# Kernel optimization log

Hardware: AMD Instinct MI355X
Metric: run time of the kernel (lower is better)

The kernel has to match this reference:

```python
import jax, jax.numpy as jnp
import numpy as np

V, E, H, B, P, Q = 100000, 300, 256, 64, 400, 50
NEG = -1e7


def _gru_param(k, s=0.08):
    k1, k2, k3, k4 = jax.random.split(k, 4)
    return (jax.random.normal(k1, (2, 3 * H, E)) * s,
            jax.random.normal(k2, (2, 3 * H, H)) * s,
            jax.random.normal(k3, (2, 3 * H)) * s,
            jax.random.normal(k4, (2, 3 * H)) * s)


def setup_inputs() -> dict:
    key = jax.random.key(0)
    ks = jax.random.split(key, 10)
    emb = (jax.random.normal(ks[0], (V, E)) * 0.1).at[0].set(0.0)  # padding_idx=0 row zeroed
    passage = jax.random.randint(ks[1], (B, P), 1, V)
    question = jax.random.randint(ks[2], (B, Q), 1, V)
    # variable lengths, padding (token 0) at the tail like pack_padded_sequence assumes
    p_len = 200 + (jnp.arange(B) * 7) % (P - 200)
    q_len = 20 + (jnp.arange(B) * 3) % (Q - 20)
    passage = jnp.where(jnp.arange(P)[None, :] < p_len[:, None], passage, 0)
    question = jnp.where(jnp.arange(Q)[None, :] < q_len[:, None], question, 0)
    pW_ih, pW_hh, pb_ih, pb_hh = _gru_param(ks[3])
    qW_ih, qW_hh, qb_ih, qb_hh = _gru_param(ks[4])
    start_w = jax.random.normal(ks[5], (6 * H,)) * 0.05
    start_b = jax.random.normal(ks[6], ()) * 0.05
    end_w = jax.random.normal(ks[7], (6 * H,)) * 0.05
    end_b = jax.random.normal(ks[8], ()) * 0.05
    return dict(passage=passage, question=question, emb=emb,
                pW_ih=pW_ih, pW_hh=pW_hh, pb_ih=pb_ih, pb_hh=pb_hh,
                qW_ih=qW_ih, qW_hh=qW_hh, qb_ih=qb_ih, qb_hh=qb_hh,
                start_w=start_w, start_b=start_b, end_w=end_w, end_b=end_b)


def bi_gru(x, mask, Wih, Whh, bih, bhh):
    """Bidirectional GRU with packed-sequence-equivalent masking.
    x: (B,T,E), mask: (B,T) float. Returns (B,T,2H). Padded outputs are 0,
    and the backward pass starts at the true last token (mask freezes state)."""
    m = mask[..., None]                                          # (B,T,1)
    xproj = jnp.einsum('bte,dhe->dbth', x, Wih) + bih[:, None, None, :]  # (2,B,T,3H)

    def run(xp, mm, Whh_d, bhh_d):
        def step(h, inp):
            xt, mt = inp                                         # (B,3H),(B,1)
            hp = h @ Whh_d.T + bhh_d
            r = jax.nn.sigmoid(xt[:, :H] + hp[:, :H])
            z = jax.nn.sigmoid(xt[:, H:2 * H] + hp[:, H:2 * H])
            n = jnp.tanh(xt[:, 2 * H:] + r * hp[:, 2 * H:])
            h_new = (1 - z) * n + z * h
            h_new = mt * h_new + (1 - mt) * h
            return h_new, h_new * mt
        h0 = jnp.zeros((xp.shape[0], H), xp.dtype)
        _, out = jax.lax.scan(step, h0, (xp.transpose(1, 0, 2), mm.transpose(1, 0, 2)))
        return out.transpose(1, 0, 2)                            # (B,T,H)

    fwd = run(xproj[0], m, Whh[0], bhh[0])
    bwd = run(xproj[1][:, ::-1], m[:, ::-1], Whh[1], bhh[1])[:, ::-1]
    return jnp.concatenate([fwd, bwd], axis=-1)


def reference(passage, question, emb,
              pW_ih, pW_hh, pb_ih, pb_hh,
              qW_ih, qW_hh, qb_ih, qb_hh,
              start_w, start_b, end_w, end_b):
    p_mask = (passage != 0).astype(jnp.float32)                  # (B,P)
    q_mask = (question != 0).astype(jnp.float32)                 # (B,Q)
    Hp = bi_gru(emb[passage], p_mask, pW_ih, pW_hh, pb_ih, pb_hh)  # (B,P,2H)
    Hq = bi_gru(emb[question], q_mask, qW_ih, qW_hh, qb_ih, qb_hh)  # (B,Q,2H)

    # Trilinear attention: decompose Linear over the cat([p, q, p*q]) terms
    w1, w2, w3 = start_w[:2 * H], start_w[2 * H:4 * H], start_w[4 * H:]
    scores = (Hp @ w1)[:, :, None] + (Hq @ w2)[:, None, :] \
        + jnp.einsum('bpd,bqd->bpq', Hp * w3, Hq) + start_b      # (B,P,Q)

    # allennlp masked_softmax: softmax(vector*mask) * mask, renormalized
    a = jax.nn.softmax(scores * q_mask[:, None, :], axis=-1) * q_mask[:, None, :]
    a = a / (a.sum(axis=-1, keepdims=True) + 1e-13)

    wavg = jnp.einsum('bpq,bqd->bpd', a, Hq)                     # (B,P,2H)
    combined = jnp.concatenate([Hp, wavg, Hp * wavg], axis=-1)   # (B,P,6H)

    start_logits = jnp.where(p_mask > 0, combined @ start_w + start_b, NEG)
    end_logits = jnp.where(p_mask > 0, combined @ end_w + end_b, NEG)
    log_mask = jnp.log(p_mask + 1e-45)
    softmax_start = jax.nn.log_softmax(start_logits + log_mask, axis=-1)
    softmax_end = jax.nn.log_softmax(end_logits + log_mask, axis=-1)
    return start_logits, end_logits, softmax_start, softmax_end
```

## Files before the change

### kernel.cpp

```cpp
#include <hip/hip_runtime.h>
#include <math.h>

constexpr int Bb = 64;
constexpr int Pp = 400;
constexpr int Qq = 50;
constexpr int Ee = 300;
constexpr int Hh = 256;
constexpr int H3 = 768;
constexpr int Dd = 512;

#define NEGC (-10000000.0f)
#define LOGTINY (-103.278929903f)

typedef _Float16 h2 __attribute__((ext_vector_type(2)));
typedef _Float16 f16x8 __attribute__((ext_vector_type(8)));
typedef float f32x4 __attribute__((ext_vector_type(4)));

__device__ __forceinline__ float allred(float v){
  #pragma unroll
  for (int off = 1; off < 64; off <<= 1) v += __shfl_xor(v, off);
  return v;
}
__device__ __forceinline__ float allmax(float v){
  #pragma unroll
  for (int off = 1; off < 64; off <<= 1) v = fmaxf(v, __shfl_xor(v, off));
  return v;
}
__device__ __forceinline__ float sigm(float x){ return 1.f / (1.f + expf(-x)); }

__device__ __forceinline__ float dot2f(unsigned a, unsigned b, float c){
#if __has_builtin(__builtin_amdgcn_fdot2)
  return __builtin_amdgcn_fdot2(__builtin_bit_cast(h2, a), __builtin_bit_cast(h2, b), c, false);
#else
  float r = c;
  asm("v_dot2_f32_f16 %0, %1, %2, %0" : "+v"(r) : "v"(a), "v"(b));
  return r;
#endif
}

#define U4C(v,c) ((c)==0?(v).x:((c)==1?(v).y:((c)==2?(v).z:(v).w)))

__global__ __launch_bounds__(256) void gather_a(const int* __restrict__ ptok,
                                                const int* __restrict__ qtok,
                                                const float* __restrict__ emb,
                                                _Float16* __restrict__ Agp,
                                                _Float16* __restrict__ Agq){
  int idx = blockIdx.x * 256 + threadIdx.x;
  if (idx >= (25600 + 3200) * 40) return;
  int ck = idx % 40;
  int row = idx / 40;
  int tokv; _Float16* dst;
  if (row < 25600){ tokv = ptok[row]; dst = Agp + (size_t)row * 320; }
  else { int r = row - 25600; tokv = qtok[r]; dst = Agq + (size_t)r * 320; }
  int c = ck * 8;
  const float* src = emb + (size_t)tokv * Ee;
  f16x8 v;
  #pragma unroll
  for (int i = 0; i < 8; ++i) v[i] = (c + i < Ee) ? (_Float16)src[c + i] : (_Float16)0.f;
  *(f16x8*)(dst + c) = v;
}

__global__ __launch_bounds__(256) void prep_wih16(const float* __restrict__ pW,
                                                  const float* __restrict__ qW,
                                                  _Float16* __restrict__ wih16){
  int idx = blockIdx.x * 256 + threadIdx.x;
  if (idx >= 2 * 2 * 768 * 160) return;
  int col2 = idx % 160;
  int r = idx / 160;
  int g = r / 1536;
  int dh = r % 1536;
  int c = col2 * 2;
  const float* W = g ? qW : pW;
  float2 v = make_float2(0.f, 0.f);
  if (c < Ee) v = *(const float2*)(W + (size_t)dh * Ee + c);
  h2 o = { (_Float16)v.x, (_Float16)v.y };
  *(h2*)(wih16 + (size_t)r * 320 + c) = o;
}

__global__ __launch_bounds__(256) void prep_w16(const float* __restrict__ pW,
                                                const float* __restrict__ qW,
                                                unsigned* __restrict__ w16){
  int idx = blockIdx.x * 256 + threadIdx.x;
  if (idx >= 393216) return;
  int c = idx & 3;
  int t = (idx >> 2) & 1023;
  int B = idx >> 12;
  int gd, g, ql;
  if (B < 28){
    gd = B / 7; int rb = B % 7;
    ql = rb / 3; g = rb % 3;
  } else if (B < 64){
    int lb0 = B - 28; gd = lb0 / 9; int lb = lb0 % 9;
    if (lb < 2){ ql = 2; g = lb + 1; }
    else if (lb < 8){ int v = lb - 2; ql = 3 + v / 3; g = v % 3; }
    else { ql = 5; g = 0; }
  } else {
    int sb0 = B - 64; gd = sb0 / 8; int sb = sb0 % 8;
    if (sb < 2){ ql = 5; g = sb + 1; }
    else { int v = sb - 2; ql = 6 + v / 3; g = v % 3; }
  }
  int j = t & 255, qq = t >> 8;
  int p = qq * 32 + ql * 4 + c;
  int row = g * 256 + j;
  int d = gd & 1, kind = gd >> 1;
  const float* W = kind ? qW : pW;
  const float* src = W + ((size_t)d * H3 + row) * Hh + 2 * p;
  _Float16 a = (_Float16)src[0], bb = (_Float16)src[1];
  unsigned short ua, ub;
  __builtin_memcpy(&ua, &a, 2); __builtin_memcpy(&ub, &bb, 2);
  w16[idx] = (unsigned)ua | ((unsigned)ub << 16);
}

__global__ __launch_bounds__(512) void xproj_mfma(const int* __restrict__ tok,
                                                  const _Float16* __restrict__ Ag,
                                                  const _Float16* __restrict__ wih16,
                                                  const float* __restrict__ bih,
                                                  _Float16* __restrict__ xp, int T){
  __shared__ __align__(16) _Float16 Af[128][72];
  __shared__ __align__(16) _Float16 Bf[128][72];
  __shared__ int anyflag;
  int tid = threadIdx.x;
  int m0 = blockIdx.y * 128;

  if (tid == 0) anyflag = 0;
  __syncthreads();
  if (tid < 128 && tok[m0 + tid] != 0) anyflag = 1;
  __syncthreads();
  if (!anyflag) return;

  int nt = blockIdx.x;
  int d = nt / 6, h0 = (nt % 6) * 128;
  int wid = tid >> 6, lane = tid & 63;
  int wr = wid >> 2, wc = wid & 3;

  int r0 = tid >> 3;
  int r1 = (tid + 512) >> 3;
  int cc = (tid & 7) * 8;
  const _Float16* eA0 = Ag + (size_t)(m0 + r0) * 320;
  const _Float16* eA1 = Ag + (size_t)(m0 + r1) * 320;
  const _Float16* wB0 = wih16 + ((size_t)d * H3 + h0 + r0) * 320;
  const _Float16* wB1 = wih16 + ((size_t)d * H3 + h0 + r1) * 320;

  f32x4 acc[4][2] = {};

  for (int k0 = 0; k0 < 320; k0 += 64){
    *(f16x8*)&Af[r0][cc] = *(const f16x8*)(eA0 + k0 + cc);
    *(f16x8*)&Af[r1][cc] = *(const f16x8*)(eA1 + k0 + cc);
    *(f16x8*)&Bf[r0][cc] = *(const f16x8*)(wB0 + k0 + cc);
    *(f16x8*)&Bf[r1][cc] = *(const f16x8*)(wB1 + k0 + cc);
    __syncthreads();
    #pragma unroll
    for (int kc = 0; kc < 2; ++kc){
      int kb = kc * 32 + (lane >> 4) * 8;
      f16x8 af[4], bf[2];
      #pragma unroll
      for (int i = 0; i < 4; ++i) af[i] = *(const f16x8*)&Af[wr * 64 + i * 16 + (lane & 15)][kb];
      #pragma unroll
      for (int jn = 0; jn < 2; ++jn) bf[jn] = *(const f16x8*)&Bf[wc * 32 + jn * 16 + (lane & 15)][kb];
      #pragma unroll
      for (int i = 0; i < 4; ++i)
        #pragma unroll
        for (int jn = 0; jn < 2; ++jn)
          acc[i][jn] = __builtin_amdgcn_mfma_f32_16x16x32_f16(af[i], bf[jn], acc[i][jn], 0, 0, 0);
    }
    __syncthreads();
  }

  #pragma unroll
  for (int jn = 0; jn < 2; ++jn){
    int h = h0 + wc * 32 + jn * 16 + (lane & 15);
    float bv = bih[d * H3 + h];
    #pragma unroll
    for (int i = 0; i < 4; ++i){
      #pragma unroll
      for (int r = 0; r < 4; ++r){
        int m = m0 + wr * 64 + i * 16 + (lane >> 4) * 4 + r;
        int bI = m / T, tI = m - bI * T;
        xp[(((size_t)d * Bb + bI) * T + tI) * H3 + h] = (_Float16)(acc[i][jn][r] + bv);
      }
    }
  }
}

__global__ __launch_bounds__(1024)
void gru_kernel(const int* __restrict__ ptok,
                const int* __restrict__ qtok,
                const _Float16* __restrict__ xpp,
                const _Float16* __restrict__ xpq,
                const unsigned* __restrict__ w16,
                const float* __restrict__ pbhh,
                const float* __restrict__ qbhh,
                float* __restrict__ Hp,
                float* __restrict__ Hq){
  int wg = blockIdx.x;
  bool isp = wg < 128;
  int lw = isp ? wg : wg - 128;
  int d = lw & 1, b = lw >> 1;
  int T = isp ? Pp : Qq;
  const int* tok = (isp ? ptok : qtok) + b * T;
  const _Float16* xrow = (isp ? xpp : xpq) + ((size_t)d * Bb + b) * T * H3;
  int gd = (isp ? 0 : 2) + d;
  const float* bhh = (isp ? pbhh : qbhh) + d * H3;
  float* Hout = (isp ? Hp : Hq) + (size_t)b * T * Dd + d * Hh;

  __shared__ __align__(16) uint4 ldsW[9 * 1024];
  __shared__ float part[3][3][Hh];
  __shared__ __align__(16) unsigned hbuf[2][128];

  int t = threadIdx.x;
  int j = t & 255, qq = t >> 8;
  const uint4* u4w = (const uint4*)w16;

  unsigned wrR[28];
  #pragma unroll
  for (int rb = 0; rb < 7; ++rb){
    uint4 v = u4w[((size_t)gd * 7 + rb) * 1024 + t];
    wrR[4 * rb + 0] = v.x; wrR[4 * rb + 1] = v.y; wrR[4 * rb + 2] = v.z; wrR[4 * rb + 3] = v.w;
  }
  #pragma unroll
  for (int i = 0; i < 28; ++i) asm volatile("" : "+v"(wrR[i]));

  #pragma unroll
  for (int lb = 0; lb < 9; ++lb)
    ldsW[lb * 1024 + t] = u4w[28 * 1024 + ((size_t)gd * 9 + lb) * 1024 + t];
  const uint4* wS = u4w + 64 * 1024 + (size_t)gd * 8 * 1024;

  float bh0 = bhh[j], bh1 = bhh[Hh + j], bh2 = bhh[2 * Hh + j];
  float h_old = 0.f;
  if (t < 128) hbuf[1][t] = 0u;
  __syncthreads();

  int t0 = d ? (T - 1) : 0;
  float pre0 = 0.f, pre1 = 0.f, pre2 = 0.f;
  if (qq == 0){
    pre0 = (float)xrow[(size_t)t0 * H3 + j];
    pre1 = (float)xrow[(size_t)t0 * H3 + Hh + j];
    pre2 = (float)xrow[(size_t)t0 * H3 + 2 * Hh + j];
  }

  for (int s = 0; s < T; ++s){
    int tt = d ? (T - 1 - s) : s;
    const uint4* hb4 = (const uint4*)&hbuf[(s + 1) & 1][qq * 32];
    float a0 = 0.f, a1 = 0.f, a2 = 0.f;

    uint4 sA0 = wS[0 * 1024 + t], sA1 = wS[1 * 1024 + t];
    uint4 sB0 = wS[2 * 1024 + t], sB1 = wS[3 * 1024 + t], sB2 = wS[4 * 1024 + t];
    uint4 sC0 = wS[5 * 1024 + t], sC1 = wS[6 * 1024 + t], sC2 = wS[7 * 1024 + t];

    #define DOT3(HQ, W0e, W1e, W2e) { _Pragma("unroll") \
      for (int c = 0; c < 4; ++c){ \
        unsigned hv = U4C(HQ, c); \
        a0 = dot2f(U4C(W0e, c), hv, a0); \
        a1 = dot2f(U4C(W1e, c), hv, a1); \
        a2 = dot2f(U4C(W2e, c), hv, a2); } }
    #define DOT1(HQ, W0e, ACC) { _Pragma("unroll") \
      for (int c = 0; c < 4; ++c){ \
        unsigned hv = U4C(HQ, c); \
        ACC = dot2f(U4C(W0e, c), hv, ACC); } }
    #define RQ(i) (*(const uint4*)&wrR[4 * (i)])

    uint4 h0q = hb4[0], h1q = hb4[1];
    DOT3(h0q, RQ(0), RQ(1), RQ(2))
    DOT3(h1q, RQ(3), RQ(4), RQ(5))
    uint4 h2q = hb4[2], h3q = hb4[3];
    DOT1(h2q, RQ(6), a0)
    { uint4 l1 = ldsW[0 * 1024 + t], l2 = ldsW[1 * 1024 + t];
      DOT1(h2q, l1, a1) DOT1(h2q, l2, a2) }
    { uint4 l0 = ldsW[2 * 1024 + t], l1 = ldsW[3 * 1024 + t], l2 = ldsW[4 * 1024 + t];
      DOT3(h3q, l0, l1, l2) }
    uint4 h4q = hb4[4], h5q = hb4[5];
    { uint4 l0 = ldsW[5 * 1024 + t], l1 = ldsW[6 * 1024 + t], l2 = ldsW[7 * 1024 + t];
      DOT3(h4q, l0, l1, l2) }
    { uint4 l0 = ldsW[8 * 1024 + t];
      DOT1(h5q, l0, a0) }
    DOT1(h5q, sA0, a1) DOT1(h5q, sA1, a2)
    uint4 h6q = hb4[6], h7q = hb4[7];
    DOT3(h6q, sB0, sB1, sB2)
    DOT3(h7q, sC0, sC1, sC2)
    #undef DOT3
    #undef DOT1
    #undef RQ

    if (qq != 0){
      part[qq - 1][0][j] = a0;
      part[qq - 1][1][j] = a1;
      part[qq - 1][2][j] = a2;
    }
    __syncthreads();
    if (qq == 0){
      float xt0 = pre0, xt1 = pre1, xt2 = pre2;
      if (s + 1 < T){
        int tn = d ? (T - 2 - s) : (s + 1);
        pre0 = (float)xrow[(size_t)tn * H3 + j];
        pre1 = (float)xrow[(size_t)tn * H3 + Hh + j];
        pre2 = (float)xrow[(size_t)tn * H3 + 2 * Hh + j];
      }
      float g0 = a0 + part[0][0][j] + part[1][0][j] + part[2][0][j] + bh0;
      float g1 = a1 + part[0][1][j] + part[1][1][j] + part[2][1][j] + bh1;
      float g2 = a2 + part[0][2][j] + part[1][2][j] + part[2][2][j] + bh2;
      float r = sigm(xt0 + g0);
      float z = sigm(xt1 + g1);
      float n = tanhf(xt2 + r * g2);
      float hnew = (1.f - z) * n + z * h_old;
      float m = (tok[tt] != 0) ? 1.f : 0.f;
      float hm = m * hnew + (1.f - m) * h_old;
      h_old = hm;
      ((_Float16*)hbuf[s & 1])[j] = (_Float16)hm;
      Hout[(size_t)tt * Dd + j] = hm * m;
    }
    __syncthreads();
  }
}

__global__ __launch_bounds__(512) void attn_kernel(const float* __restrict__ Hp,
                                                   const float* __restrict__ Hq,
                                                   const int* __restrict__ ptok,
                                                   const int* __restrict__ qtok,
                                                   const float* __restrict__ start_w,
                                                   const float* __restrict__ sbp,
                                                   const float* __restrict__ end_w,
                                                   const float* __restrict__ ebp,
                                                   float* __restrict__ out){
  extern __shared__ __align__(16) float lds[];
  float* hqs = lds;
  float* s2s = hqs + Qq * Dd;
  float* qms = s2s + 64;
  float* scw = qms + 64;
  float* aw  = scw + 512;

  int b = blockIdx.y, pc = blockIdx.x;
  int tid = threadIdx.x, wid = tid >> 6, lane = tid & 63;
  float sb = sbp[0], eb = ebp[0];

  float w1r[8], w2r[8], w3r[8], e1r[8], e2r[8], e3r[8];
  #pragma unroll
  for (int i = 0; i < 8; ++i){
    int c = lane * 8 + i;
    w1r[i] = start_w[c]; w2r[i] = start_w[Dd + c]; w3r[i] = start_w[2 * Dd + c];
    e1r[i] = end_w[c];   e2r[i] = end_w[Dd + c];   e3r[i] = end_w[2 * Dd + c];
  }
  for (int idx = tid; idx < Qq * Dd; idx += 512) hqs[idx] = Hq[(size_t)b * Qq * Dd + idx];
  __syncthreads();

  for (int q = wid; q < Qq; q += 8){
    float part = 0.f;
    const float* hq = hqs + q * Dd + lane * 8;
    #pragma unroll
    for (int i = 0; i < 8; ++i) part += hq[i] * w2r[i];
    part = allred(part);
    if (lane == 0){
      s2s[q] = part;
      qms[q] = (qtok[b * Qq + q] != 0) ? 1.f : 0.f;
    }
  }
  __syncthreads();

  for (int p = pc * 100 + wid; p < pc * 100 + 100; p += 8){
    const float* hprow = Hp + ((size_t)b * Pp + p) * Dd + lane * 8;
    float4 hv0 = *(const float4*)hprow;
    float4 hv1 = *(const float4*)(hprow + 4);
    float hpc[8] = {hv0.x, hv0.y, hv0.z, hv0.w, hv1.x, hv1.y, hv1.z, hv1.w};
    float hw3[8], he3[8];
    float s1 = 0.f, ed = 0.f;
    #pragma unroll
    for (int i = 0; i < 8; ++i){
      hw3[i] = hpc[i] * w3r[i];
      he3[i] = hpc[i] * e3r[i];
      s1 += hpc[i] * w1r[i];
      ed += hpc[i] * e1r[i];
    }
    #pragma unroll
    for (int off = 1; off < 64; off <<= 1){
      s1 += __shfl_xor(s1, off);
      ed += __shfl_xor(ed, off);
    }
    for (int q = 0; q < Qq; ++q){
      const float4* hq4 = (const float4*)(hqs + q * Dd + lane * 8);
      float4 a0 = hq4[0], a1 = hq4[1];
      float dot = hw3[0] * a0.x + hw3[1] * a0.y + hw3[2] * a0.z + hw3[3] * a0.w
                + hw3[4] * a1.x + hw3[5] * a1.y + hw3[6] * a1.z + hw3[7] * a1.w;
      dot = allred(dot);
      if (lane == 0) scw[wid * 64 + q] = (s1 + s2s[q] + dot + sb) * qms[q];
    }
    float v = (lane < Qq) ? scw[wid * 64 + lane] : -1e30f;
    float M = allmax(v);
    float ev = (lane < Qq) ? expf(v - M) : 0.f;
    float S = allred(ev);
    float am = (lane < Qq) ? (ev / S) * qms[lane] : 0.f;
    float Sm = allred(am);
    float af = am / (Sm + 1e-13f);
    if (lane < Qq) aw[wid * 64 + lane] = af;
    float wv[8] = {0.f, 0.f, 0.f, 0.f, 0.f, 0.f, 0.f, 0.f};
    for (int q = 0; q < Qq; ++q){
      float aq = aw[wid * 64 + q];
      const float4* hq4 = (const float4*)(hqs + q * Dd + lane * 8);
      float4 a0 = hq4[0], a1 = hq4[1];
      wv[0] += aq * a0.x; wv[1] += aq * a0.y; wv[2] += aq * a0.z; wv[3] += aq * a0.w;
      wv[4] += aq * a1.x; wv[5] += aq * a1.y; wv[6] += aq * a1.z; wv[7] += aq * a1.w;
    }
    float acc2 = 0.f, acc3 = 0.f, acc4 = 0.f, acc5 = 0.f;
    #pragma unroll
    for (int i = 0; i < 8; ++i){
      acc2 += wv[i] * w2r[i];
      acc3 += hw3[i] * wv[i];
      acc4 += wv[i] * e2r[i];
      acc5 += he3[i] * wv[i];
    }
    #pragma unroll
    for (int off = 1; off < 64; off <<= 1){
      acc2 += __shfl_xor(acc2, off);
      acc3 += __shfl_xor(acc3, off);
      acc4 += __shfl_xor(acc4, off);
      acc5 += __shfl_xor(acc5, off);
    }
    if (lane == 0){
      bool pm = (ptok[b * Pp + p] != 0);
      out[(size_t)b * Pp + p]                   = pm ? (s1 + acc2 + acc3 + sb) : NEGC;
      out[(size_t)Bb * Pp + (size_t)b * Pp + p] = pm ? (ed + acc4 + acc5 + eb) : NEGC;
    }
  }
}

__global__ __launch_bounds__(512) void lsm_kernel(const int* __restrict__ ptok,
                                                  float* __restrict__ out){
  int b = blockIdx.x >> 1, sel = blockIdx.x & 1;
  const float* lg = out + (size_t)sel * Bb * Pp + (size_t)b * Pp;
  float* o = out + (size_t)(2 + sel) * Bb * Pp + (size_t)b * Pp;
  int tid = threadIdx.x;
  __shared__ float red1[8];
  __shared__ float red2[8];
  float x = -1e30f;
  if (tid < Pp) x = lg[tid] + ((ptok[b * Pp + tid] != 0) ? 0.f : LOGTINY);
  float m = allmax(x);
  if ((tid & 63) == 0) red1[tid >> 6] = m;
  __syncthreads();
  float M = red1[0];
  #pragma unroll
  for (int i = 1; i < 8; ++i) M = fmaxf(M, red1[i]);
  float e = (tid < Pp) ? expf(x - M) : 0.f;
  float s = allred(e);
  if ((tid & 63) == 0) red2[tid >> 6] = s;
  __syncthreads();
  float S = 0.f;
  #pragma unroll
  for (int i = 0; i < 8; ++i) S += red2[i];
  if (tid < Pp) o[tid] = (x - M) - logf(S);
}

extern "C" void kernel_launch(void* const* d_in, const int* in_sizes, int n_in,
                              void* d_out, int out_size, void* d_ws, size_t ws_size,
                              hipStream_t stream){
  const int*   passage  = (const int*)d_in[0];
  const int*   question = (const int*)d_in[1];
  const float* emb      = (const float*)d_in[2];
  const float* pW_ih    = (const float*)d_in[3];
  const float* pW_hh    = (const float*)d_in[4];
  const float* pb_ih    = (const float*)d_in[5];
  const float* pb_hh    = (const float*)d_in[6];
  const float* qW_ih    = (const float*)d_in[7];
  const float* qW_hh    = (const float*)d_in[8];
  const float* qb_ih    = (const float*)d_in[9];
  const float* qb_hh    = (const float*)d_in[10];
  const float* start_w  = (const float*)d_in[11];
  const float* start_b  = (const float*)d_in[12];
  const float* end_w    = (const float*)d_in[13];
  const float* end_b    = (const float*)d_in[14];
  float* out = (float*)d_out;

  float*     ws    = (float*)d_ws;
  unsigned*  w16   = (unsigned*)ws;
  _Float16*  wih16 = (_Float16*)(ws + 393216);
  _Float16*  Agp   = (_Float16*)(ws + 884736);
  _Float16*  Agq   = (_Float16*)(ws + 4980736);
  _Float16*  xpp   = (_Float16*)(ws + 5492736);
  _Float16*  xpq   = (_Float16*)(ws + 25153536);
  float*     Hp    = ws + 27611136;
  float*     Hq    = ws + 40718336;

  hipLaunchKernelGGL(prep_w16, dim3(1536), dim3(256), 0, stream, pW_hh, qW_hh, w16);
  hipLaunchKernelGGL(gather_a, dim3(4500), dim3(256), 0, stream,
                     passage, question, emb, Agp, Agq);
  hipLaunchKernelGGL(prep_wih16, dim3(1920), dim3(256), 0, stream, pW_ih, qW_ih, wih16);
  hipLaunchKernelGGL(xproj_mfma, dim3(12, 200), dim3(512), 0, stream,
                     passage, Agp, wih16, pb_ih, xpp, Pp);
  hipLaunchKernelGGL(xproj_mfma, dim3(12, 25), dim3(512), 0, stream,
                     question, Agq, wih16 + (size_t)2 * H3 * 320, qb_ih, xpq, Qq);
  hipLaunchKernelGGL(gru_kernel, dim3(256), dim3(1024), 0, stream,
                     passage, question, xpp, xpq, w16, pb_hh, qb_hh, Hp, Hq);
  size_t attn_lds = (size_t)(Qq * Dd + 64 + 64 + 512 + 512) * sizeof(float);
  hipLaunchKernelGGL(attn_kernel, dim3(4, 64), dim3(512), attn_lds, stream,
                     Hp, Hq, passage, question, start_w, start_b, end_w, end_b, out);
  hipLaunchKernelGGL(lsm_kernel, dim3(128), dim3(512), 0, stream, passage, out);
}
```

Before: 892.7 us.

## Reduce GRU recurrent partial sums with wave shuffles instead of LDS and barrier

Remaps threads so the four K-quarter partial dot products for each hidden unit sit in the same wavefront, 16 lanes apart. The weight packing kernel is changed to match. The step-level reduction now uses xor shuffles instead of writing partials to LDS, taking a barrier and having one quarter of the threads finish the gates. This removes one __syncthreads and the LDS round trip per timestep. In exchange, every lane redundantly computes the gate nonlinearities and issues the xproj prefetch loads, and only 16 of 64 lanes write the output.

```diff
diff --git a/kernel.cpp b/kernel.cpp
--- a/kernel.cpp
+++ b/kernel.cpp
@@ -99,7 +99,8 @@
     if (sb < 2){ ql = 5; g = sb + 1; }
     else { int v = sb - 2; ql = 6 + v / 3; g = v % 3; }
   }
-  int j = t & 255, qq = t >> 8;
+  int l = t & 63, w = t >> 6;
+  int j = w * 16 + (l & 15), qq = l >> 4;
   int p = qq * 32 + ql * 4 + c;
   int row = g * 256 + j;
   int d = gd & 1, kind = gd >> 1;
@@ -204,11 +205,11 @@
   float* Hout = (isp ? Hp : Hq) + (size_t)b * T * Dd + d * Hh;
 
   __shared__ __align__(16) uint4 ldsW[9 * 1024];
-  __shared__ float part[3][3][Hh];
   __shared__ __align__(16) unsigned hbuf[2][128];
 
   int t = threadIdx.x;
-  int j = t & 255, qq = t >> 8;
+  int l = t & 63, w = t >> 6;
+  int j = w * 16 + (l & 15), qq = l >> 4;
   const uint4* u4w = (const uint4*)w16;
 
   unsigned wrR[28];
@@ -231,12 +232,9 @@
   __syncthreads();
 
   int t0 = d ? (T - 1) : 0;
-  float pre0 = 0.f, pre1 = 0.f, pre2 = 0.f;
-  if (qq == 0){
-    pre0 = (float)xrow[(size_t)t0 * H3 + j];
-    pre1 = (float)xrow[(size_t)t0 * H3 + Hh + j];
-    pre2 = (float)xrow[(size_t)t0 * H3 + 2 * Hh + j];
-  }
+  float pre0 = (float)xrow[(size_t)t0 * H3 + j];
+  float pre1 = (float)xrow[(size_t)t0 * H3 + Hh + j];
+  float pre2 = (float)xrow[(size_t)t0 * H3 + 2 * Hh + j];
 
   for (int s = 0; s < T; ++s){
     int tt = d ? (T - 1 - s) : s;
@@ -281,30 +279,28 @@
     #undef DOT1
     #undef RQ
 
-    if (qq != 0){
-      part[qq - 1][0][j] = a0;
-      part[qq - 1][1][j] = a1;
-      part[qq - 1][2][j] = a2;
-    }
-    __syncthreads();
-    if (qq == 0){
-      float xt0 = pre0, xt1 = pre1, xt2 = pre2;
-      if (s + 1 < T){
-        int tn = d ? (T - 2 - s) : (s + 1);
-        pre0 = (float)xrow[(size_t)tn * H3 + j];
-        pre1 = (float)xrow[(size_t)tn * H3 + Hh + j];
-        pre2 = (float)xrow[(size_t)tn * H3 + 2 * Hh + j];
-      }
-      float g0 = a0 + part[0][0][j] + part[1][0][j] + part[2][0][j] + bh0;
-      float g1 = a1 + part[0][1][j] + part[1][1][j] + part[2][1][j] + bh1;
-      float g2 = a2 + part[0][2][j] + part[1][2][j] + part[2][2][j] + bh2;
-      float r = sigm(xt0 + g0);
-      float z = sigm(xt1 + g1);
-      float n = tanhf(xt2 + r * g2);
-      float hnew = (1.f - z) * n + z * h_old;
-      float m = (tok[tt] != 0) ? 1.f : 0.f;
-      float hm = m * hnew + (1.f - m) * h_old;
-      h_old = hm;
+    a0 += __shfl_xor(a0, 16); a0 += __shfl_xor(a0, 32);
+    a1 += __shfl_xor(a1, 16); a1 += __shfl_xor(a1, 32);
+    a2 += __shfl_xor(a2, 16); a2 += __shfl_xor(a2, 32);
+
+    float xt0 = pre0, xt1 = pre1, xt2 = pre2;
+    if (s + 1 < T){
+      int tn = d ? (T - 2 - s) : (s + 1);
+      pre0 = (float)xrow[(size_t)tn * H3 + j];
+      pre1 = (float)xrow[(size_t)tn * H3 + Hh + j];
+      pre2 = (float)xrow[(size_t)tn * H3 + 2 * Hh + j];
+    }
+    float g0 = a0 + bh0;
+    float g1 = a1 + bh1;
+    float g2 = a2 + bh2;
+    float r = sigm(xt0 + g0);
+    float z = sigm(xt1 + g1);
+    float n = tanhf(xt2 + r * g2);
+    float hnew = (1.f - z) * n + z * h_old;
+    float m = (tok[tt] != 0) ? 1.f : 0.f;
+    float hm = m * hnew + (1.f - m) * h_old;
+    h_old = hm;
+    if (l < 16){
       ((_Float16*)hbuf[s & 1])[j] = (_Float16)hm;
       Hout[(size_t)tt * Dd + j] = hm * m;
     }
```

After: 1.051 ms. 17.7% more time.
